# Kernel optimization log

Hardware: AMD Instinct MI355X
Metric: run time of the kernel (lower is better)

## Reference

```python
import jax, jax.numpy as jnp
import numpy as np

EEG_CH = 64      # eeg_channel_new
WIN = 128        # window_length
KEN = 10         # cnn_ken_num
CONV_H = 64      # cnn_conv_hight (stride/kernel height)


def setup_inputs() -> dict:
    key = jax.random.key(0)
    ks = jax.random.split(key, 11)
    n = jax.random.normal
    return {
        "x": n(ks[0], (1, 1, 66, 128), dtype=jnp.float32),
        # SE fcn: Linear(64,64) -> Tanh -> Linear(64,64) -> Sigmoid -> Softmax
        "se_w1": n(ks[1], (64, 64), dtype=jnp.float32) * 0.1,
        "se_b1": n(ks[2], (64,), dtype=jnp.float32) * 0.1,
        "se_w2": n(ks[3], (64, 64), dtype=jnp.float32) * 0.1,
        "se_b2": n(ks[4], (64,), dtype=jnp.float32) * 0.1,
        # Conv2d(1, 10, (64, 9), stride=(64, 1))
        "conv_w": n(ks[5], (10, 1, 64, 9), dtype=jnp.float32) * 0.05,
        "conv_b": n(ks[6], (10,), dtype=jnp.float32) * 0.05,
        # fcn: Linear(20,10) -> Sigmoid -> Linear(10,2) -> Softmax
        "fcn_w1": n(ks[7], (10, 20), dtype=jnp.float32) * 0.1,
        "fcn_b1": n(ks[8], (10,), dtype=jnp.float32) * 0.1,
        "fcn_w2": n(ks[9], (2, 10), dtype=jnp.float32) * 0.1,
        "fcn_b2": n(ks[10], (2,), dtype=jnp.float32) * 0.1,
    }


def _dot(a, b):
    # Faithful to torch: tensordot over dim 0 -> [64,1]; diag of non-square -> [1];
    # then broadcast-divide by per-column norms -> [64].
    temp = jnp.diagonal(jnp.tensordot(a, b, axes=[[0], [0]]))  # [1]
    norm_a = jnp.linalg.norm(a, axis=0)                        # [64]
    norm_b = jnp.linalg.norm(b, axis=0)                        # [1]
    return temp / (norm_a * norm_b)                            # [64]


def reference(x, se_w1, se_b1, se_w2, se_b2, conv_w, conv_b,
              fcn_w1, fcn_b1, fcn_w2, fcn_b2):
    eeg = x[:, :, 1:1 + EEG_CH, :]      # [1,1,64,128]
    wav_a = x[:, :, 0:1, :]             # [1,1,1,128]
    wav_b = x[:, :, -1:, :]             # [1,1,1,128]

    e2 = eeg.reshape(EEG_CH, WIN)       # [64,128]
    r_a = _dot(e2.T, wav_a.reshape(1, WIN).T)   # [64]
    r_b = _dot(e2.T, wav_b.reshape(1, WIN).T)   # [64]
    eeg_r = jnp.concatenate([r_a, r_b]).reshape(2, -1)  # [2,64]

    # SE channel attention
    h = jnp.tanh(eeg_r @ se_w1.T + se_b1)
    se_w = jax.nn.softmax(jax.nn.sigmoid(h @ se_w2.T + se_b2), axis=1)  # [2,64]
    sd = eeg.reshape(1, EEG_CH, WIN).transpose(1, 0, 2)  # [64,1,128]
    sd = jnp.concatenate([sd, sd], axis=0)               # [128,1,128]
    # (transpose(0,2) * w.view(1,-1)).transpose(0,2) == scale along doubled-channel dim
    eeg_se = (sd * se_w.reshape(-1)[:, None, None]).transpose(1, 0, 2)  # [1,128,128]

    y = eeg_se.reshape(1, 1, 2 * EEG_CH, WIN)            # [1,1,128,128]
    y = jax.lax.conv_general_dilated(
        y, conv_w, window_strides=(CONV_H, 1), padding='VALID',
        dimension_numbers=('NCHW', 'OIHW', 'NCHW'))       # [1,10,2,120]
    y = jax.nn.relu(y + conv_b[None, :, None, None])
    # AdaptiveAvgPool2d((2,1)): H already 2, mean over W
    y = jnp.mean(y, axis=3, keepdims=True)                # [1,10,2,1]
    y = y.reshape(1, -1)                                  # [1,20]

    h2 = jax.nn.sigmoid(y @ fcn_w1.T + fcn_b1)
    return jax.nn.softmax(h2 @ fcn_w2.T + fcn_b2, axis=1)  # [1,2]
```

## Files before the change

kernel.cpp:

```cpp
#include <hip/hip_runtime.h>
#include <math.h>

#define EEG_CH 64
#define WIN    128
#define KW     9
#define OUTW   120
#define NOUT   10
#define ROWP   132

#define WS_SE   0
#define WS_MSUM 128

__device__ __forceinline__ float readlane_f(float v, int l) {
    return __int_as_float(__builtin_amdgcn_readlane(__float_as_int(v), l));
}

__launch_bounds__(1024)
__global__ void cnn_k1(const float* __restrict__ xg,
                       const float* __restrict__ w1g, const float* __restrict__ b1g,
                       const float* __restrict__ w2g, const float* __restrict__ b2g,
                       float* __restrict__ wsout)
{
    __shared__ float w1l[64 * 64];
    __shared__ float w2l[64 * 64];
    __shared__ float rnorm[66];
    __shared__ float nums[2];

    const int tid  = threadIdx.x;
    const int wv   = tid >> 6;
    const int lane = tid & 63;

    if (wv >= 8) {
        const bool second = (wv >= 12);
        const float* __restrict__ src = second ? w2g : w1g;
        float* __restrict__ dst = second ? w2l : w1l;
        const int t0 = (wv & 3) * 64 + lane;
        for (int t = t0; t < 1024; t += 256) {
            const int j  = t & 63;
            const int i4 = t >> 6;
            const float4 v = *(const float4*)(src + j * 64 + i4 * 4);
            dst[(i4 * 4 + 0) * 64 + j] = v.x;
            dst[(i4 * 4 + 1) * 64 + j] = v.y;
            dst[(i4 * 4 + 2) * 64 + j] = v.z;
            dst[(i4 * 4 + 3) * 64 + j] = v.w;
        }
    } else {
        for (int row = wv; row < 66; row += 8) {
            const float v0 = xg[row * WIN + lane];
            const float v1 = xg[row * WIN + 64 + lane];
            float s = v0 * v0 + v1 * v1;
            for (int off = 32; off > 0; off >>= 1) s += __shfl_xor(s, off, 64);
            if (lane == 0) rnorm[row] = sqrtf(s);
        }
        if (wv < 2) {
            const int wrow = (wv == 0) ? 0 : 65;
            float p = xg[WIN + lane]      * xg[wrow * WIN + lane]
                    + xg[WIN + 64 + lane] * xg[wrow * WIN + 64 + lane];
            for (int off = 32; off > 0; off >>= 1) p += __shfl_xor(p, off, 64);
            if (lane == 0) nums[wv] = p;
        }
    }
    __syncthreads();

    if (wv < 2) {
        const int r = wv, j = lane;
        const float er = nums[r] / (rnorm[j + 1] * (r == 0 ? rnorm[0] : rnorm[65]));
        float acc = b1g[j];
        #pragma unroll
        for (int i = 0; i < 64; ++i)
            acc += readlane_f(er, i) * w1l[i * 64 + j];
        const float hv = tanhf(acc);
        float acc2 = b2g[j];
        #pragma unroll
        for (int i = 0; i < 64; ++i)
            acc2 += readlane_f(hv, i) * w2l[i * 64 + j];
        const float sg = 1.f / (1.f + expf(-acc2));
        float mx = sg;
        for (int off = 32; off > 0; off >>= 1) mx = fmaxf(mx, __shfl_xor(mx, off, 64));
        const float e = expf(sg - mx);
        float ss = e;
        for (int off = 32; off > 0; off >>= 1) ss += __shfl_xor(ss, off, 64);
        wsout[WS_SE + r * 64 + j] = e / ss;
    }
}

__launch_bounds__(256)
__global__ void cnn_k2(const float* __restrict__ xg,
                       const float* __restrict__ cwg, const float* __restrict__ cbg,
                       float* __restrict__ wsio)
{
    __shared__ float xl[64 * ROWP];
    __shared__ float part[4][OUTW];

    const int tid  = threadIdx.x;
    const int wv   = tid >> 6;
    const int lane = tid & 63;
    const int o    = blockIdx.x;

    for (int t = tid; t < 2048; t += 256) {
        const int row = t >> 5, c4 = t & 31;
        const float4 v = *(const float4*)(xg + (row + 1) * WIN + c4 * 4);
        *(float4*)(xl + row * ROWP + c4 * 4) = v;
    }

    const int h = wv >> 1, ihalf = wv & 1;
    const int chbase = ihalf * 32;
    float wl[KW];
    float sl = 0.f;
    if (lane < 32) {
        const float* __restrict__ cwo = cwg + o * (EEG_CH * KW) + (chbase + lane) * KW;
        #pragma unroll
        for (int k = 0; k < KW; ++k) wl[k] = cwo[k];
        sl = wsio[WS_SE + h * 64 + chbase + lane];
    }
    __syncthreads();

    const int wbase = (lane < 60) ? 2 * lane : 116;
    float q0 = 0.f, q1 = 0.f;
    #pragma unroll 4
    for (int ii = 0; ii < 32; ++ii) {
        const int i = chbase + ii;
        const float2* xp = (const float2*)(xl + i * ROWP + wbase);
        const float2 x0 = xp[0], x1 = xp[1], x2 = xp[2], x3 = xp[3], x4 = xp[4];
        const float xw[10] = { x0.x, x0.y, x1.x, x1.y, x2.x, x2.y,
                               x3.x, x3.y, x4.x, x4.y };
        float wk[KW];
        #pragma unroll
        for (int k = 0; k < KW; ++k) wk[k] = readlane_f(wl[k], ii);
        const float s = readlane_f(sl, ii);
        float p0 = 0.f, p1 = 0.f;
        #pragma unroll
        for (int k = 0; k < KW; ++k) {
            p0 += xw[k]     * wk[k];
            p1 += xw[k + 1] * wk[k];
        }
        q0 += s * p0;
        q1 += s * p1;
    }
    if (lane < 60) {
        *(float2*)(&part[wv][wbase]) = make_float2(q0, q1);
    }
    __syncthreads();

    if (wv < 2) {
        const float bo = cbg[o];
        float r = 0.f;
        if (lane < 60) {
            const float v0 = part[wv * 2][wbase]     + part[wv * 2 + 1][wbase]     + bo;
            const float v1 = part[wv * 2][wbase + 1] + part[wv * 2 + 1][wbase + 1] + bo;
            r = fmaxf(v0, 0.f) + fmaxf(v1, 0.f);
        }
        for (int off = 32; off > 0; off >>= 1) r += __shfl_xor(r, off, 64);
        if (lane == 0) wsio[WS_MSUM + o * 2 + wv] = r * (1.0f / OUTW);
    }
}

__launch_bounds__(64)
__global__ void cnn_k3(const float* __restrict__ wsin,
                       const float* __restrict__ f1w, const float* __restrict__ f1b,
                       const float* __restrict__ f2w, const float* __restrict__ f2b,
                       float* __restrict__ out)
{
    const int lane = threadIdx.x;
    float h2v = 0.f;
    if (lane < 10) {
        float a = f1b[lane];
        #pragma unroll
        for (int p = 0; p < 20; ++p) a += wsin[WS_MSUM + p] * f1w[lane * 20 + p];
        h2v = 1.f / (1.f + expf(-a));
    }
    float t0 = (lane < 10) ? h2v * f2w[lane]      : 0.f;
    float t1 = (lane < 10) ? h2v * f2w[10 + lane] : 0.f;
    for (int off = 32; off > 0; off >>= 1) {
        t0 += __shfl_xor(t0, off, 64);
        t1 += __shfl_xor(t1, off, 64);
    }
    if (lane == 0) {
        const float l0 = f2b[0] + t0, l1 = f2b[1] + t1;
        const float m  = fmaxf(l0, l1);
        const float e0 = expf(l0 - m), e1 = expf(l1 - m);
        out[0] = e0 / (e0 + e1);
        out[1] = e1 / (e0 + e1);
    }
}

extern "C" void kernel_launch(void* const* d_in, const int* in_sizes, int n_in,
                              void* d_out, int out_size, void* d_ws, size_t ws_size,
                              hipStream_t stream) {
    (void)in_sizes; (void)n_in; (void)ws_size; (void)out_size;
    const float* xg  = (const float*)d_in[0];
    const float* w1  = (const float*)d_in[1];
    const float* b1  = (const float*)d_in[2];
    const float* w2  = (const float*)d_in[3];
    const float* b2  = (const float*)d_in[4];
    const float* cw  = (const float*)d_in[5];
    const float* cb  = (const float*)d_in[6];
    const float* f1w = (const float*)d_in[7];
    const float* f1b = (const float*)d_in[8];
    const float* f2w = (const float*)d_in[9];
    const float* f2b = (const float*)d_in[10];
    float* out = (float*)d_out;
    float* wsf = (float*)d_ws;

    cnn_k1<<<dim3(1),    dim3(1024), 0, stream>>>(xg, w1, b1, w2, b2, wsf);
    cnn_k2<<<dim3(NOUT), dim3(256),  0, stream>>>(xg, cw, cb, wsf);
    cnn_k3<<<dim3(1),    dim3(64),   0, stream>>>(wsf, f1w, f1b, f2w, f2b, out);
}
```

Before: 88.66 us.

## Fuse three kernels into one with redundant SE compute and last-block finish

Merges the SE-attention, convolution and final FCN kernels into a single launch. Each of the 10 blocks recomputes the SE weights redundantly in shared memory, which removes the dependency on a separate launch. The last block to arrive, detected through a global atomic counter, runs the small FCN and softmax. This trades two kernel launch gaps for redundant work per block and a larger shared-memory footprint.

```diff
diff --git a/kernel.cpp b/kernel.cpp
--- a/kernel.cpp
+++ b/kernel.cpp
@@ -8,57 +8,75 @@
 #define NOUT   10
 #define ROWP   132
 
-#define WS_SE   0
-#define WS_MSUM 128
+__device__ float        g_msum[2 * NOUT];
+__device__ unsigned int g_ctr = 0;
 
 __device__ __forceinline__ float readlane_f(float v, int l) {
     return __int_as_float(__builtin_amdgcn_readlane(__float_as_int(v), l));
 }
 
-__launch_bounds__(1024)
-__global__ void cnn_k1(const float* __restrict__ xg,
-                       const float* __restrict__ w1g, const float* __restrict__ b1g,
-                       const float* __restrict__ w2g, const float* __restrict__ b2g,
-                       float* __restrict__ wsout)
+__launch_bounds__(256)
+__global__ void cnn_fused(const float* __restrict__ xg,
+                          const float* __restrict__ w1g, const float* __restrict__ b1g,
+                          const float* __restrict__ w2g, const float* __restrict__ b2g,
+                          const float* __restrict__ cwg, const float* __restrict__ cbg,
+                          const float* __restrict__ f1w, const float* __restrict__ f1b,
+                          const float* __restrict__ f2w, const float* __restrict__ f2b,
+                          float* __restrict__ out)
 {
     __shared__ float w1l[64 * 64];
     __shared__ float w2l[64 * 64];
+    __shared__ float xl[64 * ROWP];
     __shared__ float rnorm[66];
     __shared__ float nums[2];
+    __shared__ float sef[128];
+    __shared__ float part[4][OUTW];
+    __shared__ float msh[2];
+    __shared__ int   sflag;
+    __shared__ float msums[2 * NOUT];
 
     const int tid  = threadIdx.x;
     const int wv   = tid >> 6;
     const int lane = tid & 63;
-
-    if (wv >= 8) {
-        const bool second = (wv >= 12);
-        const float* __restrict__ src = second ? w2g : w1g;
-        float* __restrict__ dst = second ? w2l : w1l;
-        const int t0 = (wv & 3) * 64 + lane;
-        for (int t = t0; t < 1024; t += 256) {
-            const int j  = t & 63;
-            const int i4 = t >> 6;
-            const float4 v = *(const float4*)(src + j * 64 + i4 * 4);
-            dst[(i4 * 4 + 0) * 64 + j] = v.x;
-            dst[(i4 * 4 + 1) * 64 + j] = v.y;
-            dst[(i4 * 4 + 2) * 64 + j] = v.z;
-            dst[(i4 * 4 + 3) * 64 + j] = v.w;
-        }
-    } else {
-        for (int row = wv; row < 66; row += 8) {
-            const float v0 = xg[row * WIN + lane];
-            const float v1 = xg[row * WIN + 64 + lane];
-            float s = v0 * v0 + v1 * v1;
-            for (int off = 32; off > 0; off >>= 1) s += __shfl_xor(s, off, 64);
-            if (lane == 0) rnorm[row] = sqrtf(s);
-        }
-        if (wv < 2) {
-            const int wrow = (wv == 0) ? 0 : 65;
-            float p = xg[WIN + lane]      * xg[wrow * WIN + lane]
-                    + xg[WIN + 64 + lane] * xg[wrow * WIN + 64 + lane];
-            for (int off = 32; off > 0; off >>= 1) p += __shfl_xor(p, off, 64);
-            if (lane == 0) nums[wv] = p;
-        }
+    const int o    = blockIdx.x;
+
+    for (int t = tid; t < 2048; t += 256) {
+        const int row = t >> 5, c4 = t & 31;
+        const float4 v = *(const float4*)(xg + (row + 1) * WIN + c4 * 4);
+        *(float4*)(xl + row * ROWP + c4 * 4) = v;
+    }
+    for (int t = tid; t < 2048; t += 256) {
+        const int j  = t & 63;
+        const int i4 = (t >> 6) & 15;
+        const float* __restrict__ src = (t < 1024) ? w1g : w2g;
+        float* __restrict__ dst = (t < 1024) ? w1l : w2l;
+        const float4 v = *(const float4*)(src + j * 64 + i4 * 4);
+        dst[(i4 * 4 + 0) * 64 + j] = v.x;
+        dst[(i4 * 4 + 1) * 64 + j] = v.y;
+        dst[(i4 * 4 + 2) * 64 + j] = v.z;
+        dst[(i4 * 4 + 3) * 64 + j] = v.w;
+    }
+    const int h = wv >> 1, ihalf = wv & 1;
+    const int chbase = ihalf * 32;
+    float wl[KW];
+    if (lane < 32) {
+        const float* __restrict__ cwo = cwg + o * (EEG_CH * KW) + (chbase + lane) * KW;
+        #pragma unroll
+        for (int k = 0; k < KW; ++k) wl[k] = cwo[k];
+    }
+    for (int row = wv; row < 66; row += 4) {
+        const float v0 = xg[row * WIN + lane];
+        const float v1 = xg[row * WIN + 64 + lane];
+        float s = v0 * v0 + v1 * v1;
+        for (int off = 32; off > 0; off >>= 1) s += __shfl_xor(s, off, 64);
+        if (lane == 0) rnorm[row] = sqrtf(s);
+    }
+    if (wv < 2) {
+        const int wrow = (wv == 0) ? 0 : 65;
+        float p = xg[WIN + lane]      * xg[wrow * WIN + lane]
+                + xg[WIN + 64 + lane] * xg[wrow * WIN + 64 + lane];
+        for (int off = 32; off > 0; off >>= 1) p += __shfl_xor(p, off, 64);
+        if (lane == 0) nums[wv] = p;
     }
     __syncthreads();
 
@@ -80,40 +98,12 @@
         const float e = expf(sg - mx);
         float ss = e;
         for (int off = 32; off > 0; off >>= 1) ss += __shfl_xor(ss, off, 64);
-        wsout[WS_SE + r * 64 + j] = e / ss;
-    }
-}
-
-__launch_bounds__(256)
-__global__ void cnn_k2(const float* __restrict__ xg,
-                       const float* __restrict__ cwg, const float* __restrict__ cbg,
-                       float* __restrict__ wsio)
-{
-    __shared__ float xl[64 * ROWP];
-    __shared__ float part[4][OUTW];
-
-    const int tid  = threadIdx.x;
-    const int wv   = tid >> 6;
-    const int lane = tid & 63;
-    const int o    = blockIdx.x;
-
-    for (int t = tid; t < 2048; t += 256) {
-        const int row = t >> 5, c4 = t & 31;
-        const float4 v = *(const float4*)(xg + (row + 1) * WIN + c4 * 4);
-        *(float4*)(xl + row * ROWP + c4 * 4) = v;
-    }
-
-    const int h = wv >> 1, ihalf = wv & 1;
-    const int chbase = ihalf * 32;
-    float wl[KW];
+        sef[r * 64 + j] = e / ss;
+    }
+    __syncthreads();
+
     float sl = 0.f;
-    if (lane < 32) {
-        const float* __restrict__ cwo = cwg + o * (EEG_CH * KW) + (chbase + lane) * KW;
-        #pragma unroll
-        for (int k = 0; k < KW; ++k) wl[k] = cwo[k];
-        sl = wsio[WS_SE + h * 64 + chbase + lane];
-    }
-    __syncthreads();
+    if (lane < 32) sl = sef[h * 64 + chbase + lane];
 
     const int wbase = (lane < 60) ? 2 * lane : 116;
     float q0 = 0.f, q1 = 0.f;
@@ -151,43 +141,51 @@
             r = fmaxf(v0, 0.f) + fmaxf(v1, 0.f);
         }
         for (int off = 32; off > 0; off >>= 1) r += __shfl_xor(r, off, 64);
-        if (lane == 0) wsio[WS_MSUM + o * 2 + wv] = r * (1.0f / OUTW);
-    }
-}
-
-__launch_bounds__(64)
-__global__ void cnn_k3(const float* __restrict__ wsin,
-                       const float* __restrict__ f1w, const float* __restrict__ f1b,
-                       const float* __restrict__ f2w, const float* __restrict__ f2b,
-                       float* __restrict__ out)
-{
-    const int lane = threadIdx.x;
-    float h2v = 0.f;
-    if (lane < 10) {
-        float a = f1b[lane];
-        #pragma unroll
-        for (int p = 0; p < 20; ++p) a += wsin[WS_MSUM + p] * f1w[lane * 20 + p];
-        h2v = 1.f / (1.f + expf(-a));
-    }
-    float t0 = (lane < 10) ? h2v * f2w[lane]      : 0.f;
-    float t1 = (lane < 10) ? h2v * f2w[10 + lane] : 0.f;
-    for (int off = 32; off > 0; off >>= 1) {
-        t0 += __shfl_xor(t0, off, 64);
-        t1 += __shfl_xor(t1, off, 64);
-    }
-    if (lane == 0) {
-        const float l0 = f2b[0] + t0, l1 = f2b[1] + t1;
-        const float m  = fmaxf(l0, l1);
-        const float e0 = expf(l0 - m), e1 = expf(l1 - m);
-        out[0] = e0 / (e0 + e1);
-        out[1] = e1 / (e0 + e1);
+        if (lane == 0) msh[wv] = r * (1.0f / OUTW);
+    }
+    __syncthreads();
+
+    if (tid == 0) {
+        __hip_atomic_store(&g_msum[o * 2 + 0], msh[0], __ATOMIC_RELAXED, __HIP_MEMORY_SCOPE_AGENT);
+        __hip_atomic_store(&g_msum[o * 2 + 1], msh[1], __ATOMIC_RELAXED, __HIP_MEMORY_SCOPE_AGENT);
+        const unsigned old = __hip_atomic_fetch_add(&g_ctr, 1u, __ATOMIC_ACQ_REL, __HIP_MEMORY_SCOPE_AGENT);
+        sflag = (old % 10u == 9u) ? 1 : 0;
+    }
+    __syncthreads();
+
+    if (sflag) {
+        if (tid < 2 * NOUT)
+            msums[tid] = __hip_atomic_load(&g_msum[tid], __ATOMIC_ACQUIRE, __HIP_MEMORY_SCOPE_AGENT);
+        __syncthreads();
+        if (tid < 64) {
+            float h2v = 0.f;
+            if (lane < 10) {
+                float a = f1b[lane];
+                #pragma unroll
+                for (int p = 0; p < 20; ++p) a += msums[p] * f1w[lane * 20 + p];
+                h2v = 1.f / (1.f + expf(-a));
+            }
+            float t0 = (lane < 10) ? h2v * f2w[lane]      : 0.f;
+            float t1 = (lane < 10) ? h2v * f2w[10 + lane] : 0.f;
+            for (int off = 32; off > 0; off >>= 1) {
+                t0 += __shfl_xor(t0, off, 64);
+                t1 += __shfl_xor(t1, off, 64);
+            }
+            if (lane == 0) {
+                const float l0 = f2b[0] + t0, l1 = f2b[1] + t1;
+                const float m  = fmaxf(l0, l1);
+                const float e0 = expf(l0 - m), e1 = expf(l1 - m);
+                out[0] = e0 / (e0 + e1);
+                out[1] = e1 / (e0 + e1);
+            }
+        }
     }
 }
 
 extern "C" void kernel_launch(void* const* d_in, const int* in_sizes, int n_in,
                               void* d_out, int out_size, void* d_ws, size_t ws_size,
                               hipStream_t stream) {
-    (void)in_sizes; (void)n_in; (void)ws_size; (void)out_size;
+    (void)in_sizes; (void)n_in; (void)ws_size; (void)out_size; (void)d_ws;
     const float* xg  = (const float*)d_in[0];
     const float* w1  = (const float*)d_in[1];
     const float* b1  = (const float*)d_in[2];
@@ -200,9 +198,7 @@
     const float* f2w = (const float*)d_in[9];
     const float* f2b = (const float*)d_in[10];
     float* out = (float*)d_out;
-    float* wsf = (float*)d_ws;
-
-    cnn_k1<<<dim3(1),    dim3(1024), 0, stream>>>(xg, w1, b1, w2, b2, wsf);
-    cnn_k2<<<dim3(NOUT), dim3(256),  0, stream>>>(xg, cw, cb, wsf);
-    cnn_k3<<<dim3(1),    dim3(64),   0, stream>>>(wsf, f1w, f1b, f2w, f2b, out);
+
+    cnn_fused<<<dim3(NOUT), dim3(256), 0, stream>>>(xg, w1, b1, w2, b2,
+                                                    cw, cb, f1w, f1b, f2w, f2b, out);
 }
```

After: 91.05 us. 1.03x slower.
